# Optimization experiments

Hardware: AMD Instinct MI355X
Metric: run time of the kernel (lower is better)

Reference implementation:

```python
import jax, jax.numpy as jnp
import numpy as np

N, H, W = 8, 64, 64
CIN = 512    # latent_size_prev == conv_insize
COUT = 512   # latent_size == conv_outsize
Z = 512      # latent vector dim


def setup_inputs() -> dict:
    key = jax.random.key(0)
    ks = jax.random.split(key, 6)
    data = jax.random.normal(ks[0], (N, H, W, CIN), dtype=jnp.float32)
    latent = jax.random.normal(ks[1], (N, Z), dtype=jnp.float32)
    dense_w = jax.random.normal(ks[2], (Z, CIN), dtype=jnp.float32)
    dense_b = jnp.ones((CIN,), dtype=jnp.float32)  # ones_initializer per StyleBlock2
    conv_w = jax.random.normal(ks[3], (3, 3, CIN, COUT), dtype=jnp.float32)
    bias = jnp.zeros((1, 1, 1, COUT), dtype=jnp.float32)
    noise_coef = jnp.zeros((1, 1, 1, COUT), dtype=jnp.float32)
    noise = jax.random.normal(ks[4], (N, H, W, COUT), dtype=jnp.float32)
    return {"data": data, "latent": latent, "dense_w": dense_w, "dense_b": dense_b,
            "conv_w": conv_w, "bias": bias, "noise_coef": noise_coef, "noise": noise}


def reference(data, latent, dense_w, dense_b, conv_w, bias, noise_coef, noise):
    # ScaledDense: style vector s = latent @ (W * sqrt(2/Z)) + b
    dense_coef = jnp.sqrt(2.0 / Z).astype(data.dtype)
    s = latent @ (dense_w * dense_coef) + dense_b           # [N, CIN]

    # modulate input by style
    x = data * s[:, None, None, :]                          # [N,H,W,CIN]

    conv_coef = jnp.sqrt(2.0 / (CIN * 9)).astype(data.dtype)
    w = conv_w * conv_coef                                  # [3,3,CIN,COUT]
    y = jax.lax.conv_general_dilated(
        x, w, window_strides=(1, 1), padding='SAME',
        dimension_numbers=('NHWC', 'HWIO', 'NHWC'))         # [N,H,W,COUT]

    # demodulation: sum_{k,k,cin} (w * s)^2 == (s^2) @ sum_{k,k} w^2
    w2 = jnp.sum(w * w, axis=(0, 1))                        # [CIN, COUT]
    d = jax.lax.rsqrt((s * s) @ w2 + 1e-8)                  # [N, COUT]
    y = y * d[:, None, None, :]

    y = y + bias + noise * noise_coef
    return jnp.where(y >= 0, y, 0.2 * y)  # leaky relu, alpha=0.2
```

## Files before the change

### kernel.cpp

```cpp
#include <hip/hip_runtime.h>
#include <stdint.h>

typedef unsigned short ushort_t;
typedef unsigned int uint_t;
typedef __bf16 bf16x8 __attribute__((ext_vector_type(8)));
typedef float f32x4 __attribute__((ext_vector_type(4)));

#define C2F 0.02083333333333333f

__device__ __forceinline__ float bf2f(unsigned short u) {
  union { unsigned int i; float f; } v; v.i = ((unsigned int)u) << 16; return v.f;
}
__device__ __forceinline__ unsigned short f2bf(float f) {
  union { float f; unsigned int i; } v; v.f = f;
  unsigned int r = v.i + 0x7FFFu + ((v.i >> 16) & 1u);
  return (unsigned short)(r >> 16);
}
__device__ __forceinline__ bool bf_mode(const void* dense_b) {
  return *(const uint_t*)dense_b == 0x3F803F80u;
}
__device__ __forceinline__ void async16(const void* g, void* l) {
  __builtin_amdgcn_global_load_lds(
      (const __attribute__((address_space(1))) unsigned int*)g,
      (__attribute__((address_space(3))) unsigned int*)l, 16, 0, 0);
}

__global__ void k_style_p(const void* __restrict__ latent, const void* __restrict__ dw,
                          const void* __restrict__ db, float* __restrict__ sp) {
  const bool bf = bf_mode(db);
  int c = blockIdx.x * 256 + threadIdx.x;
  int n = blockIdx.y, zc = blockIdx.z;
  int z0 = zc * 64;
  float acc = 0.f;
  if (bf) {
    const ushort_t* L = (const ushort_t*)latent;
    const ushort_t* W = (const ushort_t*)dw;
    for (int z = z0; z < z0 + 64; ++z) acc += bf2f(L[n * 512 + z]) * bf2f(W[z * 512 + c]);
  } else {
    const float* L = (const float*)latent;
    const float* W = (const float*)dw;
    for (int z = z0; z < z0 + 64; ++z) acc += L[n * 512 + z] * W[z * 512 + c];
  }
  sp[(zc * 8 + n) * 512 + c] = acc;
}

__global__ void k_style_f(const float* __restrict__ sp, const void* __restrict__ db,
                          float* __restrict__ s) {
  const bool bf = bf_mode(db);
  int c = blockIdx.x * 256 + threadIdx.x;
  int n = blockIdx.y;
  float acc = 0.f;
#pragma unroll
  for (int zc = 0; zc < 8; ++zc) acc += sp[(zc * 8 + n) * 512 + c];
  float bv = bf ? bf2f(((const ushort_t*)db)[c]) : ((const float*)db)[c];
  s[n * 512 + c] = acc * 0.0625f + bv;
}

__global__ void k_w2(const void* __restrict__ cw, const void* __restrict__ db,
                     float* __restrict__ w2) {
  const bool bf = bf_mode(db);
  int i = blockIdx.x * blockDim.x + threadIdx.x;
  float a = 0.f;
  if (bf) {
    const ushort_t* W = (const ushort_t*)cw;
    for (int t = 0; t < 9; ++t) { float v = bf2f(W[t * 262144 + i]); a += v * v; }
  } else {
    const float* W = (const float*)cw;
    for (int t = 0; t < 9; ++t) { float v = W[t * 262144 + i]; a += v * v; }
  }
  w2[i] = a;
}

__global__ void k_demod_p(const float* __restrict__ s, const float* __restrict__ w2,
                          float* __restrict__ qp) {
  int c = blockIdx.x * 256 + threadIdx.x;
  int n = blockIdx.y, kc = blockIdx.z;
  int k0 = kc * 64;
  float q = 0.f;
  for (int k = k0; k < k0 + 64; ++k) {
    float sv = s[n * 512 + k];
    q += sv * sv * w2[k * 512 + c];
  }
  qp[(kc * 8 + n) * 512 + c] = q;
}

__global__ void k_demod_f(const float* __restrict__ qp, float* __restrict__ dfac) {
  int c = blockIdx.x * 256 + threadIdx.x;
  int n = blockIdx.y;
  float q = 0.f;
#pragma unroll
  for (int kc = 0; kc < 8; ++kc) q += qp[(kc * 8 + n) * 512 + c];
  dfac[n * 512 + c] = C2F * rsqrtf(C2F * C2F * q + 1e-8f);
}

__global__ void k_wt(const void* __restrict__ cw, const void* __restrict__ db,
                     ushort_t* __restrict__ wT) {
  __shared__ ushort_t tile[64][66];
  const bool bf = bf_mode(db);
  int tap = blockIdx.z;
  int ci0 = blockIdx.y * 64, co0 = blockIdx.x * 64;
  int col = threadIdx.x & 63, r0 = threadIdx.x >> 6;
  if (bf) {
    const ushort_t* src = (const ushort_t*)cw + tap * 262144;
    for (int r = r0; r < 64; r += 4) tile[r][col] = src[(ci0 + r) * 512 + co0 + col];
  } else {
    const float* src = (const float*)cw + tap * 262144;
    for (int r = r0; r < 64; r += 4) tile[r][col] = f2bf(src[(ci0 + r) * 512 + co0 + col]);
  }
  __syncthreads();
  ushort_t* dst = wT + tap * 262144;
  for (int r = r0; r < 64; r += 4)
    dst[(co0 + r) * 512 + ci0 + col] = tile[col][r];
}

__global__ void k_xpad(const void* __restrict__ data, const void* __restrict__ db,
                       const float* __restrict__ s, ushort_t* __restrict__ xpad) {
  const bool bf = bf_mode(db);
  int idx = blockIdx.x * 256 + threadIdx.x;
  int c = (idx & 63) * 8;
  int p = idx >> 6;
  int wp = p % 66; int q = p / 66; int hp = q % 66; int n = q / 66;
  uint_t ov[4] = {0u, 0u, 0u, 0u};
  if ((unsigned)(hp - 1) < 64u && (unsigned)(wp - 1) < 64u) {
    const float4 s0 = *(const float4*)(s + n * 512 + c);
    const float4 s1 = *(const float4*)(s + n * 512 + c + 4);
    size_t src = (size_t)((n * 64 + (hp - 1)) * 64 + (wp - 1)) * 512 + c;
    float x[8];
    if (bf) {
      uint4 dv = *(const uint4*)((const ushort_t*)data + src);
      x[0] = bf2f((unsigned short)(dv.x & 0xFFFFu)); x[1] = bf2f((unsigned short)(dv.x >> 16));
      x[2] = bf2f((unsigned short)(dv.y & 0xFFFFu)); x[3] = bf2f((unsigned short)(dv.y >> 16));
      x[4] = bf2f((unsigned short)(dv.z & 0xFFFFu)); x[5] = bf2f((unsigned short)(dv.z >> 16));
      x[6] = bf2f((unsigned short)(dv.w & 0xFFFFu)); x[7] = bf2f((unsigned short)(dv.w >> 16));
    } else {
      const float* df = (const float*)data + src;
      float4 a = *(const float4*)df; float4 b = *(const float4*)(df + 4);
      x[0] = a.x; x[1] = a.y; x[2] = a.z; x[3] = a.w;
      x[4] = b.x; x[5] = b.y; x[6] = b.z; x[7] = b.w;
    }
    float sv[8] = {s0.x, s0.y, s0.z, s0.w, s1.x, s1.y, s1.z, s1.w};
#pragma unroll
    for (int j = 0; j < 4; ++j)
      ov[j] = (uint_t)f2bf(x[j * 2] * sv[j * 2]) |
              ((uint_t)f2bf(x[j * 2 + 1] * sv[j * 2 + 1]) << 16);
  }
  uint4 o; o.x = ov[0]; o.y = ov[1]; o.z = ov[2]; o.w = ov[3];
  *(uint4*)(xpad + (size_t)p * 512 + c) = o;
}

template <bool BF>
__device__ __forceinline__ void epi(
    const f32x4 (&acc)[2][4][2][2], const float* __restrict__ dfac,
    const void* __restrict__ bias, const void* __restrict__ ncoef,
    const void* __restrict__ noise, void* __restrict__ out,
    int n_img, int posBase, int coutBase, int lane, int wr, int wc) {
  const int rq = (lane >> 4) * 4;
#pragma unroll
  for (int nh = 0; nh < 2; ++nh)
#pragma unroll
  for (int fn = 0; fn < 2; ++fn) {
    const int cout = coutBase + wc * 64 + nh * 32 + fn * 16 + (lane & 15);
    const float dv = dfac[n_img * 512 + cout];
    const float bv = BF ? bf2f(((const ushort_t*)bias)[cout]) : ((const float*)bias)[cout];
    const float nc = BF ? bf2f(((const ushort_t*)ncoef)[cout]) : ((const float*)ncoef)[cout];
#pragma unroll
    for (int mh = 0; mh < 2; ++mh)
#pragma unroll
    for (int f = 0; f < 4; ++f) {
      const int m = wr * 128 + mh * 64 + f * 16 + rq;
#pragma unroll
      for (int r = 0; r < 4; ++r) {
        const size_t o = (size_t)(posBase + m + r) * 512 + cout;
        const float nv = BF ? bf2f(((const ushort_t*)noise)[o]) : ((const float*)noise)[o];
        float y = acc[mh][f][nh][fn][r] * dv + bv + nv * nc;
        y = (y >= 0.f) ? y : 0.2f * y;
        if (BF) ((ushort_t*)out)[o] = f2bf(y);
        else    ((float*)out)[o] = y;
      }
    }
  }
}

__global__ __launch_bounds__(512, 2) void k_conv(
    const ushort_t* __restrict__ xpad, const ushort_t* __restrict__ wT,
    const float* __restrict__ dfac, const void* __restrict__ bias,
    const void* __restrict__ ncoef, const void* __restrict__ noise,
    const void* __restrict__ db, void* __restrict__ out) {
  extern __shared__ ushort_t lds[];

  const int t = threadIdx.x;
  const int bid = blockIdx.x;
  const int coutBase = (bid & 1) * 256;
  const int posBase = (bid >> 1) * 256;
  const int n_img = posBase >> 12;
  const int hh0 = (posBase >> 6) & 63;

  const int rt = t >> 3;
  const int c8 = ((t & 7) ^ (rt & 7)) * 8;
  const ushort_t* aPtr = xpad + ((size_t)((n_img * 66 + hh0) * 66 + rt) * 512 + c8);
  const int bRow = ((t >> 8) & 1) * 64 + ((t >> 3) & 31);
  const ushort_t* bPtr = wT + ((size_t)(coutBase + bRow) * 512 + c8);
  ushort_t* aLds = lds + t * 8;
  ushort_t* bLds = lds + 32768 + t * 8;

#define STG_A(slot, mh, kt) do { \
    const int tap_ = (kt) >> 3, kh_ = tap_ / 3, kw_ = tap_ - kh_ * 3, k0_ = ((kt) & 7) << 6; \
    async16(aPtr + ((((mh) + kh_) * 66 + kw_) * 512 + k0_), \
            aLds + (slot) * 16384 + (mh) * 4096); \
    async16(aPtr + ((((mh) + 2 + kh_) * 66 + kw_) * 512 + k0_), \
            aLds + (slot) * 16384 + ((mh) + 2) * 4096); \
  } while (0)
#define STG_B(slot, nh, kt) do { \
    const int tap_ = (kt) >> 3, k0_ = ((kt) & 7) << 6; \
    async16(bPtr + (tap_ * 262144 + (nh) * 16384 + k0_), \
            bLds + (slot) * 16384 + (nh) * 8192); \
    async16(bPtr + (tap_ * 262144 + (nh) * 16384 + 65536 + k0_), \
            bLds + (slot) * 16384 + (nh) * 8192 + 4096); \
  } while (0)

  STG_A(0, 0, 0); STG_B(0, 0, 0); STG_B(0, 1, 0); STG_A(0, 1, 0);
  STG_A(1, 0, 1); STG_B(1, 0, 1); STG_B(1, 1, 1);

  const int lane = t & 63, wid = t >> 6, wr = wid >> 2, wc = wid & 3;
  const int g16 = (lane >> 4) * 16, lrow = lane & 15, xv = (lane & 7) << 4;
  const char* LB = (const char*)lds;
  const int sbA0 = (((wr * 128 + lrow) * 128) + g16) ^ xv;
  const int sbA1 = (((wr * 128 + lrow) * 128) + 64 + g16) ^ xv;
  const int sbB0 = ((65536 + (wc * 32 + lrow) * 128) + g16) ^ xv;
  const int sbB1 = ((65536 + (wc * 32 + lrow) * 128) + 64 + g16) ^ xv;

  bf16x8 rA[4][2], rB0[2][2], rB1[2][2];
  f32x4 acc[2][4][2][2] = {};

#define LDA(mh, sB) do { _Pragma("unroll") for (int f = 0; f < 4; ++f) { \
    rA[f][0] = *(const bf16x8*)(LB + ((sB) + (mh) * 8192 + f * 2048 + sbA0)); \
    rA[f][1] = *(const bf16x8*)(LB + ((sB) + (mh) * 8192 + f * 2048 + sbA1)); } } while (0)
#define LDB(R, nh, sB) do { _Pragma("unroll") for (int fn = 0; fn < 2; ++fn) { \
    R[fn][0] = *(const bf16x8*)(LB + ((sB) + (nh) * 16384 + fn * 2048 + sbB0)); \
    R[fn][1] = *(const bf16x8*)(LB + ((sB) + (nh) * 16384 + fn * 2048 + sbB1)); } } while (0)
#define MM(mh, nh, RB) do { __builtin_amdgcn_s_setprio(1); \
    _Pragma("unroll") for (int f = 0; f < 4; ++f) \
    _Pragma("unroll") for (int fn = 0; fn < 2; ++fn) \
    _Pragma("unroll") for (int ks = 0; ks < 2; ++ks) \
      acc[mh][f][nh][fn] = __builtin_amdgcn_mfma_f32_16x16x32_bf16( \
          rA[f][ks], (RB)[fn][ks], acc[mh][f][nh][fn], 0, 0, 0); \
    __builtin_amdgcn_s_setprio(0); } while (0)
#define BAR()   asm volatile("s_barrier" ::: "memory")
#define LGKM0() asm volatile("s_waitcnt lgkmcnt(0)" ::: "memory")
#define WAITV6() asm volatile("s_waitcnt vmcnt(6)" ::: "memory")

  WAITV6();
  BAR();

#pragma unroll 1
  for (int it = 0; it < 36; ++it) {
    const int kt0 = 2 * it;
    const int ktA = kt0 + 1;
    const int ktB = (kt0 + 2 <= 71) ? kt0 + 2 : 71;
    const int ktC = (kt0 + 3 <= 71) ? kt0 + 3 : 71;
    LDA(0, 0); LDB(rB0, 0, 0);
    STG_A(1, 1, ktA);
    BAR(); LGKM0(); MM(0, 0, rB0); BAR();
    LDB(rB1, 1, 0);
    STG_A(0, 0, ktB);
    BAR(); LGKM0(); MM(0, 1, rB1); BAR();
    LDA(1, 0);
    STG_B(0, 0, ktB);
    BAR(); LGKM0(); MM(1, 1, rB1); BAR();
    STG_B(0, 1, ktB);
    BAR(); MM(1, 0, rB0); WAITV6(); BAR();
    LDA(0, 32768); LDB(rB0, 0, 32768);
    STG_A(0, 1, ktB);
    BAR(); LGKM0(); MM(0, 0, rB0); BAR();
    LDB(rB1, 1, 32768);
    STG_A(1, 0, ktC);
    BAR(); LGKM0(); MM(0, 1, rB1); BAR();
    LDA(1, 32768);
    STG_B(1, 0, ktC);
    BAR(); LGKM0(); MM(1, 1, rB1); BAR();
    STG_B(1, 1, ktC);
    BAR(); MM(1, 0, rB0); WAITV6(); BAR();
  }
  asm volatile("s_waitcnt vmcnt(0)" ::: "memory");

  if (bf_mode(db))
    epi<true>(acc, dfac, bias, ncoef, noise, out, n_img, posBase, coutBase, lane, wr, wc);
  else
    epi<false>(acc, dfac, bias, ncoef, noise, out, n_img, posBase, coutBase, lane, wr, wc);
#undef STG_A
#undef STG_B
#undef LDA
#undef LDB
#undef MM
#undef BAR
#undef LGKM0
#undef WAITV6
}

extern "C" void kernel_launch(void* const* d_in, const int* in_sizes, int n_in,
                              void* d_out, int out_size, void* d_ws, size_t ws_size,
                              hipStream_t stream) {
  (void)in_sizes; (void)n_in; (void)out_size; (void)ws_size;
  const void* data    = d_in[0];
  const void* latent  = d_in[1];
  const void* dense_w = d_in[2];
  const void* dense_b = d_in[3];
  const void* conv_w  = d_in[4];
  const void* bias    = d_in[5];
  const void* ncoef   = d_in[6];
  const void* noise   = d_in[7];

  static int once = [] {
    (void)hipFuncSetAttribute((const void*)k_conv,
                              hipFuncAttributeMaxDynamicSharedMemorySize, 131072);
    return 0;
  }();
  (void)once;

  float* s    = (float*)d_ws;
  float* dfac = s + 4096;
  float* w2   = dfac + 4096;
  float* sp   = w2 + 262144;
  float* qp   = sp + 32768;
  ushort_t* wT   = (ushort_t*)(qp + 32768);
  ushort_t* xpad = wT + 2359296;

  k_style_p<<<dim3(2, 8, 8), 256, 0, stream>>>(latent, dense_w, dense_b, sp);
  k_style_f<<<dim3(2, 8), 256, 0, stream>>>(sp, dense_b, s);
  k_w2<<<1024, 256, 0, stream>>>(conv_w, dense_b, w2);
  k_wt<<<dim3(8, 8, 9), 256, 0, stream>>>(conv_w, dense_b, wT);
  k_demod_p<<<dim3(2, 8, 8), 256, 0, stream>>>(s, w2, qp);
  k_demod_f<<<dim3(2, 8), 256, 0, stream>>>(qp, dfac);
  k_xpad<<<8712, 256, 0, stream>>>(data, dense_b, s, xpad);
  k_conv<<<256, 512, 131072, stream>>>(xpad, wT, dfac, bias, ncoef, noise, dense_b, d_out);
}
```

Before: 397.7 us.

## Restructure conv main loop to one barrier per stage and remap block order

Rewrites the pipelined main loop of the implicit-GEMM conv. Each stage now has a single barrier instead of two, the LDS fragment loads are hoisted ahead of the loop, and global loads are waited on with vmcnt(4) instead of vmcnt(6). It also remaps block indices so that consecutive launched blocks are spread across spatial tiles, which changes cache and XCD locality. The aim is to cut synchronisation stalls and overlap LDS reads with MFMA work, at the risk of LDS buffer races if the reordered stages overwrite data that is still being read.

New measurement: 389.7 us. 1.02x faster.

```diff
diff --git a/kernel.cpp b/kernel.cpp
--- a/kernel.cpp
+++ b/kernel.cpp
@@ -189,7 +189,8 @@
   extern __shared__ ushort_t lds[];
 
   const int t = threadIdx.x;
-  const int bid = blockIdx.x;
+  const int bid0 = blockIdx.x;
+  const int bid = (bid0 & 7) * 32 + (bid0 >> 3);
   const int coutBase = (bid & 1) * 256;
   const int posBase = (bid >> 1) * 256;
   const int n_img = posBase >> 12;
@@ -245,12 +246,15 @@
       acc[mh][f][nh][fn] = __builtin_amdgcn_mfma_f32_16x16x32_bf16( \
           rA[f][ks], (RB)[fn][ks], acc[mh][f][nh][fn], 0, 0, 0); \
     __builtin_amdgcn_s_setprio(0); } while (0)
-#define BAR()   asm volatile("s_barrier" ::: "memory")
-#define LGKM0() asm volatile("s_waitcnt lgkmcnt(0)" ::: "memory")
+#define BAR()   __builtin_amdgcn_s_barrier()
+#define LGKM0() do { asm volatile("s_waitcnt lgkmcnt(0)" ::: "memory"); \
+    __builtin_amdgcn_sched_barrier(0); } while (0)
+#define WAITV4() asm volatile("s_waitcnt vmcnt(4)" ::: "memory")
 #define WAITV6() asm volatile("s_waitcnt vmcnt(6)" ::: "memory")
 
   WAITV6();
   BAR();
+  LDA(0, 0); LDB(rB0, 0, 0);
 
 #pragma unroll 1
   for (int it = 0; it < 36; ++it) {
@@ -258,28 +262,30 @@
     const int ktA = kt0 + 1;
     const int ktB = (kt0 + 2 <= 71) ? kt0 + 2 : 71;
     const int ktC = (kt0 + 3 <= 71) ? kt0 + 3 : 71;
+    LGKM0(); MM(0, 0, rB0);
+    LDB(rB1, 1, 0);
+    STG_A(1, 1, ktA); BAR();
+    LGKM0(); MM(0, 1, rB1);
+    LDA(1, 0);
+    STG_A(0, 0, ktB); BAR();
+    LGKM0(); MM(1, 1, rB1);
+    STG_B(0, 0, ktB); BAR();
+    MM(1, 0, rB0);
+    WAITV4();
+    LDA(0, 32768); LDB(rB0, 0, 32768);
+    STG_B(0, 1, ktB); BAR();
+    LGKM0(); MM(0, 0, rB0);
+    LDB(rB1, 1, 32768);
+    STG_A(0, 1, ktB); BAR();
+    LGKM0(); MM(0, 1, rB1);
+    LDA(1, 32768);
+    STG_A(1, 0, ktC); BAR();
+    LGKM0(); MM(1, 1, rB1);
+    STG_B(1, 0, ktC); BAR();
+    MM(1, 0, rB0);
+    WAITV4();
     LDA(0, 0); LDB(rB0, 0, 0);
-    STG_A(1, 1, ktA);
-    BAR(); LGKM0(); MM(0, 0, rB0); BAR();
-    LDB(rB1, 1, 0);
-    STG_A(0, 0, ktB);
-    BAR(); LGKM0(); MM(0, 1, rB1); BAR();
-    LDA(1, 0);
-    STG_B(0, 0, ktB);
-    BAR(); LGKM0(); MM(1, 1, rB1); BAR();
-    STG_B(0, 1, ktB);
-    BAR(); MM(1, 0, rB0); WAITV6(); BAR();
-    LDA(0, 32768); LDB(rB0, 0, 32768);
-    STG_A(0, 1, ktB);
-    BAR(); LGKM0(); MM(0, 0, rB0); BAR();
-    LDB(rB1, 1, 32768);
-    STG_A(1, 0, ktC);
-    BAR(); LGKM0(); MM(0, 1, rB1); BAR();
-    LDA(1, 32768);
-    STG_B(1, 0, ktC);
-    BAR(); LGKM0(); MM(1, 1, rB1); BAR();
-    STG_B(1, 1, ktC);
-    BAR(); MM(1, 0, rB0); WAITV6(); BAR();
+    STG_B(1, 1, ktC); BAR();
   }
   asm volatile("s_waitcnt vmcnt(0)" ::: "memory");
 
@@ -294,6 +300,7 @@
 #undef MM
 #undef BAR
 #undef LGKM0
+#undef WAITV4
 #undef WAITV6
 }
 
```

## Double-buffer LDS fragments across MFMA phases, reorder K loop, remap blocks

Applied to the files above, without the earlier changes.

Restructures the conv main loop so that LDS fragment loads for the next MFMA phase are issued before the current MFMA block. Extra register sets (rA2, rB0a/b) allow this, and per-phase lgkmcnt(0) waits and one barrier per phase are removed in favor of vmcnt waits and sched_barrier. The K iteration order changes to channel-chunk-major with taps inner, and block IDs are remapped so blocks sharing an image/weights run concurrently. This risks higher register pressure at 2 blocks/CU, and it relies on compiler-inserted waits for LDS read correctness.

New measurement: 387.1 us. -2.7%, faster.

```diff
diff --git a/kernel.cpp b/kernel.cpp
--- a/kernel.cpp
+++ b/kernel.cpp
@@ -189,7 +189,8 @@
   extern __shared__ ushort_t lds[];
 
   const int t = threadIdx.x;
-  const int bid = blockIdx.x;
+  const int bid0 = blockIdx.x;
+  const int bid = (bid0 & 7) * 32 + (bid0 >> 3);
   const int coutBase = (bid & 1) * 256;
   const int posBase = (bid >> 1) * 256;
   const int n_img = posBase >> 12;
@@ -204,18 +205,25 @@
   ushort_t* bLds = lds + 32768 + t * 8;
 
 #define STG_A(slot, mh, kt) do { \
-    const int tap_ = (kt) >> 3, kh_ = tap_ / 3, kw_ = tap_ - kh_ * 3, k0_ = ((kt) & 7) << 6; \
-    async16(aPtr + ((((mh) + kh_) * 66 + kw_) * 512 + k0_), \
-            aLds + (slot) * 16384 + (mh) * 4096); \
-    async16(aPtr + ((((mh) + 2 + kh_) * 66 + kw_) * 512 + k0_), \
-            aLds + (slot) * 16384 + ((mh) + 2) * 4096); \
+    const int cc_ = (kt) / 9, tap_ = (kt) - cc_ * 9; \
+    const int kh_ = tap_ / 3, kw_ = tap_ - kh_ * 3; \
+    const int ko_ = (kh_ * 66 + kw_) * 512 + cc_ * 64; \
+    async16(aPtr + (ko_ + 0), aLds + (slot) * 16384 + (mh) * 4096); \
+    async16(aPtr + (ko_ + 2 * 33792), aLds + (slot) * 16384 + ((mh) + 2) * 4096); \
   } while (0)
 #define STG_B(slot, nh, kt) do { \
-    const int tap_ = (kt) >> 3, k0_ = ((kt) & 7) << 6; \
-    async16(bPtr + (tap_ * 262144 + (nh) * 16384 + k0_), \
-            bLds + (slot) * 16384 + (nh) * 8192); \
-    async16(bPtr + (tap_ * 262144 + (nh) * 16384 + 65536 + k0_), \
-            bLds + (slot) * 16384 + (nh) * 8192 + 4096); \
+    const int cc_ = (kt) / 9, tap_ = (kt) - cc_ * 9; \
+    const int ko_ = tap_ * 262144 + cc_ * 64; \
+    async16(bPtr + (ko_ + (nh) * 16384), bLds + (slot) * 16384 + (nh) * 8192); \
+    async16(bPtr + (ko_ + (nh) * 16384 + 65536), bLds + (slot) * 16384 + (nh) * 8192 + 4096); \
+  } while (0)
+#undef STG_A
+#define STG_A(slot, mh, kt) do { \
+    const int cc_ = (kt) / 9, tap_ = (kt) - cc_ * 9; \
+    const int kh_ = tap_ / 3, kw_ = tap_ - kh_ * 3; \
+    const int ko_ = (kh_ * 66 + kw_) * 512 + cc_ * 64; \
+    async16(aPtr + (ko_ + (mh) * 33792), aLds + (slot) * 16384 + (mh) * 4096); \
+    async16(aPtr + (ko_ + ((mh) + 2) * 33792), aLds + (slot) * 16384 + ((mh) + 2) * 4096); \
   } while (0)
 
   STG_A(0, 0, 0); STG_B(0, 0, 0); STG_B(0, 1, 0); STG_A(0, 1, 0);
@@ -229,28 +237,30 @@
   const int sbB0 = ((65536 + (wc * 32 + lrow) * 128) + g16) ^ xv;
   const int sbB1 = ((65536 + (wc * 32 + lrow) * 128) + 64 + g16) ^ xv;
 
-  bf16x8 rA[4][2], rB0[2][2], rB1[2][2];
+  bf16x8 rA[4][2], rA2[4][2], rB0a[2][2], rB0b[2][2], rB1[2][2];
   f32x4 acc[2][4][2][2] = {};
 
-#define LDA(mh, sB) do { _Pragma("unroll") for (int f = 0; f < 4; ++f) { \
-    rA[f][0] = *(const bf16x8*)(LB + ((sB) + (mh) * 8192 + f * 2048 + sbA0)); \
-    rA[f][1] = *(const bf16x8*)(LB + ((sB) + (mh) * 8192 + f * 2048 + sbA1)); } } while (0)
+#define LDA(R, mh, sB) do { _Pragma("unroll") for (int f = 0; f < 4; ++f) { \
+    R[f][0] = *(const bf16x8*)(LB + ((sB) + (mh) * 8192 + f * 2048 + sbA0)); \
+    R[f][1] = *(const bf16x8*)(LB + ((sB) + (mh) * 8192 + f * 2048 + sbA1)); } } while (0)
 #define LDB(R, nh, sB) do { _Pragma("unroll") for (int fn = 0; fn < 2; ++fn) { \
     R[fn][0] = *(const bf16x8*)(LB + ((sB) + (nh) * 16384 + fn * 2048 + sbB0)); \
     R[fn][1] = *(const bf16x8*)(LB + ((sB) + (nh) * 16384 + fn * 2048 + sbB1)); } } while (0)
-#define MM(mh, nh, RB) do { __builtin_amdgcn_s_setprio(1); \
+#define MM(mh, nh, RA, RB) do { __builtin_amdgcn_s_setprio(1); \
     _Pragma("unroll") for (int f = 0; f < 4; ++f) \
     _Pragma("unroll") for (int fn = 0; fn < 2; ++fn) \
     _Pragma("unroll") for (int ks = 0; ks < 2; ++ks) \
       acc[mh][f][nh][fn] = __builtin_amdgcn_mfma_f32_16x16x32_bf16( \
-          rA[f][ks], (RB)[fn][ks], acc[mh][f][nh][fn], 0, 0, 0); \
+          (RA)[f][ks], (RB)[fn][ks], acc[mh][f][nh][fn], 0, 0, 0); \
     __builtin_amdgcn_s_setprio(0); } while (0)
-#define BAR()   asm volatile("s_barrier" ::: "memory")
-#define LGKM0() asm volatile("s_waitcnt lgkmcnt(0)" ::: "memory")
+#define BAR()    __builtin_amdgcn_s_barrier()
+#define SCHED()  __builtin_amdgcn_sched_barrier(0)
 #define WAITV6() asm volatile("s_waitcnt vmcnt(6)" ::: "memory")
+#define WAITV8() asm volatile("s_waitcnt vmcnt(8)" ::: "memory")
 
   WAITV6();
   BAR();
+  LDA(rA, 0, 0); LDB(rB0a, 0, 0);
 
 #pragma unroll 1
   for (int it = 0; it < 36; ++it) {
@@ -258,28 +268,38 @@
     const int ktA = kt0 + 1;
     const int ktB = (kt0 + 2 <= 71) ? kt0 + 2 : 71;
     const int ktC = (kt0 + 3 <= 71) ? kt0 + 3 : 71;
-    LDA(0, 0); LDB(rB0, 0, 0);
+    WAITV8();
+    LDB(rB1, 1, 0);
     STG_A(1, 1, ktA);
-    BAR(); LGKM0(); MM(0, 0, rB0); BAR();
-    LDB(rB1, 1, 0);
+    SCHED(); MM(0, 0, rA, rB0a); BAR();
+    WAITV8();
+    LDA(rA2, 1, 0);
     STG_A(0, 0, ktB);
-    BAR(); LGKM0(); MM(0, 1, rB1); BAR();
-    LDA(1, 0);
+    SCHED(); MM(0, 1, rA, rB1); BAR();
+    WAITV8();
+    LDA(rA, 0, 32768);
     STG_B(0, 0, ktB);
-    BAR(); LGKM0(); MM(1, 1, rB1); BAR();
+    SCHED(); MM(1, 1, rA2, rB1); BAR();
+    WAITV8();
+    LDB(rB0b, 0, 32768);
     STG_B(0, 1, ktB);
-    BAR(); MM(1, 0, rB0); WAITV6(); BAR();
-    LDA(0, 32768); LDB(rB0, 0, 32768);
+    SCHED(); MM(1, 0, rA2, rB0a); BAR();
+    WAITV8();
+    LDB(rB1, 1, 32768);
     STG_A(0, 1, ktB);
-    BAR(); LGKM0(); MM(0, 0, rB0); BAR();
-    LDB(rB1, 1, 32768);
+    SCHED(); MM(0, 0, rA, rB0b); BAR();
+    WAITV8();
+    LDA(rA2, 1, 32768);
     STG_A(1, 0, ktC);
-    BAR(); LGKM0(); MM(0, 1, rB1); BAR();
-    LDA(1, 32768);
+    SCHED(); MM(0, 1, rA, rB1); BAR();
+    WAITV8();
+    LDA(rA, 0, 0);
     STG_B(1, 0, ktC);
-    BAR(); LGKM0(); MM(1, 1, rB1); BAR();
+    SCHED(); MM(1, 1, rA2, rB1); BAR();
+    WAITV8();
+    LDB(rB0a, 0, 0);
     STG_B(1, 1, ktC);
-    BAR(); MM(1, 0, rB0); WAITV6(); BAR();
+    SCHED(); MM(1, 0, rA2, rB0b); BAR();
   }
   asm volatile("s_waitcnt vmcnt(0)" ::: "memory");
 
@@ -293,8 +313,9 @@
 #undef LDB
 #undef MM
 #undef BAR
-#undef LGKM0
+#undef SCHED
 #undef WAITV6
+#undef WAITV8
 }
 
 extern "C" void kernel_launch(void* const* d_in, const int* in_sizes, int n_in,
```
